# Performance work log

Hardware: AMD Instinct MI355X
Metric: run time of the kernel (lower is better)

Reference implementation:

```python
import jax, jax.numpy as jnp
import numpy as np

H = 8           # attention heads
SPARSITY = 0.5  # fraction of keys kept per query row

def _silu(x):
    return x * jax.nn.sigmoid(x)

def _forward(x_t, t, te_w1, te_b1, te_w2, te_b2, fe_w1, fe_b1, fe_w2, fe_b2,
             fp_w1, fp_b1, fp_w2, fp_b2, fp_w3, fp_b3, fid_emb,
             wq, bq, wk, bk, wv, bv, wo, bo,
             gp_w1, gp_b1, gp_w2, gp_b2, ln_g, ln_b,
             dn_w1, dn_b1, dn_w2, dn_b2, dn_w3, dn_b3):
    B, F = x_t.shape
    D = te_w1.shape[1]
    hd = D // H
    # time / feature embeddings (Linear-SiLU-Linear)
    t_emb = _silu(t[:, None] @ te_w1 + te_b1) @ te_w2 + te_b2        # [B, D]
    x_emb = _silu(x_t @ fe_w1 + fe_b1) @ fe_w2 + fe_b2               # [B, D]
    comb = jnp.concatenate([
        jnp.broadcast_to(x_emb[:, None, :], (B, F, D)),
        jnp.broadcast_to(t_emb[:, None, :], (B, F, D))], axis=-1)    # [B, F, 2D]
    # shared per-feature processor (n_features > 32 branch)
    h = _silu(comb @ fp_w1 + fp_b1)
    h = _silu(h @ fp_w2 + fp_b2)
    h = h @ fp_w3 + fp_b3                                            # [B, F, D]
    d4 = fid_emb.shape[1]
    fid_pad = jnp.concatenate([fid_emb, jnp.zeros((F, D - d4), h.dtype)], axis=-1)
    feats = h + 0.1 * fid_pad[None]                                  # [B, F, D]
    # sparse feature attention (dropout is identity in eval)
    def split(x):
        return x.reshape(B, F, H, hd).transpose(0, 2, 1, 3)          # [B, H, F, hd]
    q = split(feats @ wq + bq)
    k = split(feats @ wk + bk)
    v = split(feats @ wv + bv)
    scores = jnp.einsum('bhqd,bhkd->bhqk', q, k) / (hd ** 0.5)
    k_value = max(1, int(F * SPARSITY))
    thr = jax.lax.top_k(scores, k_value)[0][..., -1:]                # kth largest per row
    scores = jnp.where(scores < thr, -1e9, scores)                   # masked_fill(-1e9)
    attn = jax.nn.softmax(scores, axis=-1)
    out = jnp.einsum('bhqk,bhkd->bhqd', attn, v)
    out = out.transpose(0, 2, 1, 3).reshape(B, F, D) @ wo + bo       # [B, F, D]
    # global pooling + processor with LayerNorm (eps=1e-5)
    g = out.mean(axis=1)
    g = _silu(g @ gp_w1 + gp_b1) @ gp_w2 + gp_b2
    mu = g.mean(-1, keepdims=True)
    var = ((g - mu) ** 2).mean(-1, keepdims=True)
    g = (g - mu) / jnp.sqrt(var + 1e-5) * ln_g + ln_b
    # denoise net -> tanh of mean half
    r = _silu(g @ dn_w1 + dn_b1)
    r = _silu(r @ dn_w2 + dn_b2)
    r = r @ dn_w3 + dn_b3                                            # [B, 2F]
    return jnp.tanh(r[:, :F])

def setup_inputs():
    B, F, D = 512, 128, 512
    D4 = D // 4
    ks = iter(jax.random.split(jax.random.key(0), 40))
    def w(shape):
        return jax.random.normal(next(ks), shape, jnp.float32) / np.sqrt(shape[0]).astype(np.float32)
    z = lambda n: jnp.zeros((n,), jnp.float32)
    return dict(
        x_t=jax.random.normal(next(ks), (B, F), jnp.float32),
        t=jax.random.uniform(next(ks), (B,), jnp.float32),
        te_w1=w((1, D)), te_b1=z(D), te_w2=w((D, D)), te_b2=z(D),
        fe_w1=w((F, D)), fe_b1=z(D), fe_w2=w((D, D)), fe_b2=z(D),
        fp_w1=w((2 * D, D)), fp_b1=z(D), fp_w2=w((D, D)), fp_b2=z(D),
        fp_w3=w((D, D)), fp_b3=z(D),
        fid_emb=jax.random.normal(next(ks), (F, D4), jnp.float32),
        wq=w((D, D)), bq=z(D), wk=w((D, D)), bk=z(D),
        wv=w((D, D)), bv=z(D), wo=w((D, D)), bo=z(D),
        gp_w1=w((D, 2 * D)), gp_b1=z(2 * D), gp_w2=w((2 * D, D)), gp_b2=z(D),
        ln_g=jnp.ones((D,), jnp.float32), ln_b=z(D),
        dn_w1=w((D, 2 * D)), dn_b1=z(2 * D), dn_w2=w((2 * D, 2 * D)), dn_b2=z(2 * D),
        dn_w3=w((2 * D, 2 * F)), dn_b3=z(2 * F),
    )

def reference(x_t, t, te_w1, te_b1, te_w2, te_b2, fe_w1, fe_b1, fe_w2, fe_b2,
              fp_w1, fp_b1, fp_w2, fp_b2, fp_w3, fp_b3, fid_emb,
              wq, bq, wk, bk, wv, bv, wo, bo,
              gp_w1, gp_b1, gp_w2, gp_b2, ln_g, ln_b,
              dn_w1, dn_b1, dn_w2, dn_b2, dn_w3, dn_b3):
    return _forward(x_t, t, te_w1, te_b1, te_w2, te_b2, fe_w1, fe_b1, fe_w2, fe_b2,
                    fp_w1, fp_b1, fp_w2, fp_b2, fp_w3, fp_b3, fid_emb,
                    wq, bq, wk, bk, wv, bv, wo, bo,
                    gp_w1, gp_b1, gp_w2, gp_b2, ln_g, ln_b,
                    dn_w1, dn_b1, dn_w2, dn_b2, dn_w3, dn_b3)
```

## Files before the change

kernel.cpp:

```cpp
#include <hip/hip_runtime.h>

__device__ __forceinline__ float silu_f(float x) { return x / (1.f + __expf(-x)); }

struct AOp {
  const float* P;
  const float* w1;
  const float* b0;
  int lda;
  int tgen;
};

template <int NPROB, int T1GEN>
__global__ __launch_bounds__(256) void gemm_p(
    AOp a0, AOp a1,
    const float* __restrict__ B0, const float* __restrict__ B1,
    const float* __restrict__ B2, int ldb,
    float* __restrict__ O0, float* __restrict__ O1, float* __restrict__ O2,
    int ldc, int Kslab, int ls, long slabMN) {
  __shared__ float As[2][32][68];
  __shared__ float Bs[2][32][68];
  const int tid = threadIdx.x;
  const int z = blockIdx.z;
  const int zi = (NPROB > 1) ? (z >> ls) : 0;
  const int s  = (NPROB > 1) ? (z & ((1 << ls) - 1)) : z;
  const AOp a = (NPROB > 1 && zi == 1) ? a1 : a0;
  const float* Bp = ((NPROB > 2 && zi == 2) ? B2 : (zi == 1) ? B1 : B0)
                    + (long)(s * Kslab) * ldb;
  float* Obase = ((NPROB > 2 && zi == 2) ? O2 : (zi == 1) ? O1 : O0)
                 + (long)s * slabMN;
  const int kbase = s * Kslab;
  const long bm = blockIdx.y * 64, bn = blockIdx.x * 64;
  const int tg = T1GEN ? a.tgen : 0;

  float acc[4][4] = {};
  const int ar = tid >> 3;
  const int ak = (tid & 7) << 2;
  const int br = tid >> 4;
  const int bn4 = (tid & 15) << 2;
  const int ty = tid >> 4, tx = tid & 15;

  float4 rA[2];
  float4 rB[2];
  float4 rW, rC;
  float tm0 = 0.f, tm1 = 0.f;

  auto loadA = [&](int k0) {
    int kg = kbase + k0 + ak;
    if (T1GEN && tg) {
      rW = *(const float4*)&a.w1[kg];
      rC = *(const float4*)&a.b0[kg];
    } else {
#pragma unroll
      for (int h = 0; h < 2; ++h)
        rA[h] = *(const float4*)&a.P[(bm + ar + h * 32) * (long)a.lda + kg];
    }
  };
  auto loadB = [&](int k0) {
#pragma unroll
    for (int h = 0; h < 2; ++h)
      rB[h] = *(const float4*)&Bp[(long)(k0 + br + h * 16) * ldb + bn + bn4];
  };
  auto store = [&](int buf) {
#pragma unroll
    for (int h = 0; h < 2; ++h) {
      int m = ar + h * 32;
      float4 av;
      if (T1GEN && tg) {
        float tm = h ? tm1 : tm0;
        av.x = silu_f(tm * rW.x + rC.x);
        av.y = silu_f(tm * rW.y + rC.y);
        av.z = silu_f(tm * rW.z + rC.z);
        av.w = silu_f(tm * rW.w + rC.w);
      } else {
        av = rA[h];
      }
      As[buf][ak + 0][m] = av.x; As[buf][ak + 1][m] = av.y;
      As[buf][ak + 2][m] = av.z; As[buf][ak + 3][m] = av.w;
    }
#pragma unroll
    for (int h = 0; h < 2; ++h) *(float4*)&Bs[buf][br + h * 16][bn4] = rB[h];
  };

  if (T1GEN && tg) { tm0 = a.P[bm + ar]; tm1 = a.P[bm + ar + 32]; }
  loadA(0); loadB(0);
  store(0);
  if (32 < Kslab) { loadA(32); loadB(32); }

  int cur = 0;
  for (int k0 = 0; k0 < Kslab; k0 += 32) {
    __syncthreads();
    if (k0 + 32 < Kslab) store(cur ^ 1);
    if (k0 + 64 < Kslab) { loadA(k0 + 64); loadB(k0 + 64); }
#pragma unroll
    for (int k = 0; k < 32; ++k) {
      float4 a4 = *(const float4*)&As[cur][k][ty << 2];
      float4 b4 = *(const float4*)&Bs[cur][k][tx << 2];
      float am[4] = {a4.x, a4.y, a4.z, a4.w};
      float bv[4] = {b4.x, b4.y, b4.z, b4.w};
#pragma unroll
      for (int i = 0; i < 4; ++i)
#pragma unroll
        for (int j = 0; j < 4; ++j) acc[i][j] = fmaf(am[i], bv[j], acc[i][j]);
    }
    cur ^= 1;
  }

  float* O = Obase + (bm + ty * 4) * (long)ldc + bn + tx * 4;
#pragma unroll
  for (int i = 0; i < 4; ++i) {
    float4 v = {acc[i][0], acc[i][1], acc[i][2], acc[i][3]};
    *(float4*)&O[(long)i * ldc] = v;
  }
}

__global__ __launch_bounds__(256) void gemm_bt(
    const float* __restrict__ A, int lda, const float* __restrict__ B, int ldb,
    float* __restrict__ OUT, int ldc, int K, float alpha,
    int zAoff, int zBoff, int zCoff) {
  __shared__ float As[2][32][68];
  __shared__ float Bs[2][32][68];
  const int tid = threadIdx.x;
  const int z = blockIdx.z;
  const long bm = blockIdx.y * 64, bn = blockIdx.x * 64;
  const float* Ab = A + (long)z * zAoff;
  const float* Bp = B + (long)z * zBoff;
  float* Obase = OUT + (long)z * zCoff;
  float acc[4][4] = {};
  const int ar = tid >> 3;
  const int ak = (tid & 7) << 2;
  const int ty = tid >> 4, tx = tid & 15;
  float4 rA[2], rB[2];
  auto loadAB = [&](int k0) {
#pragma unroll
    for (int h = 0; h < 2; ++h) {
      rA[h] = *(const float4*)&Ab[(bm + ar + h * 32) * (long)lda + k0 + ak];
      rB[h] = *(const float4*)&Bp[(bn + ar + h * 32) * (long)ldb + k0 + ak];
    }
  };
  auto store = [&](int buf) {
#pragma unroll
    for (int h = 0; h < 2; ++h) {
      int m = ar + h * 32;
      As[buf][ak + 0][m] = rA[h].x; As[buf][ak + 1][m] = rA[h].y;
      As[buf][ak + 2][m] = rA[h].z; As[buf][ak + 3][m] = rA[h].w;
      Bs[buf][ak + 0][m] = rB[h].x; Bs[buf][ak + 1][m] = rB[h].y;
      Bs[buf][ak + 2][m] = rB[h].z; Bs[buf][ak + 3][m] = rB[h].w;
    }
  };
  loadAB(0); store(0);
  if (32 < K) loadAB(32);
  int cur = 0;
  for (int k0 = 0; k0 < K; k0 += 32) {
    __syncthreads();
    if (k0 + 32 < K) store(cur ^ 1);
    if (k0 + 64 < K) loadAB(k0 + 64);
#pragma unroll
    for (int k = 0; k < 32; ++k) {
      float4 a4 = *(const float4*)&As[cur][k][ty << 2];
      float4 b4 = *(const float4*)&Bs[cur][k][tx << 2];
      float am[4] = {a4.x, a4.y, a4.z, a4.w};
      float bv[4] = {b4.x, b4.y, b4.z, b4.w};
#pragma unroll
      for (int i = 0; i < 4; ++i)
#pragma unroll
        for (int j = 0; j < 4; ++j) acc[i][j] = fmaf(am[i], bv[j], acc[i][j]);
    }
    cur ^= 1;
  }
  float* O = Obase + (bm + ty * 4) * (long)ldc + bn + tx * 4;
#pragma unroll
  for (int i = 0; i < 4; ++i) {
    float4 v = {alpha * acc[i][0], alpha * acc[i][1], alpha * acc[i][2],
                alpha * acc[i][3]};
    *(float4*)&O[(long)i * ldc] = v;
  }
}

template <int NS, int ACT>
__global__ __launch_bounds__(256) void sumk(
    const float* __restrict__ P, long slabMN,
    const float* __restrict__ b0, const float* __restrict__ b1, int bsplit,
    int cmask, float* __restrict__ out) {
  int i4 = (blockIdx.x * 256 + threadIdx.x) << 2;
  float4 s = *(const float4*)&P[i4];
#pragma unroll
  for (int si = 1; si < NS; ++si) {
    float4 p = *(const float4*)&P[(long)si * slabMN + i4];
    s.x += p.x; s.y += p.y; s.z += p.z; s.w += p.w;
  }
  int c = i4 & cmask;
  const float* bp = (b1 && c >= bsplit) ? (b1 + c - bsplit) : (b0 + c);
  float4 bb = *(const float4*)bp;
  s.x += bb.x; s.y += bb.y; s.z += bb.z; s.w += bb.w;
  if (ACT == 1) {
    s.x = silu_f(s.x); s.y = silu_f(s.y); s.z = silu_f(s.z); s.w = silu_f(s.w);
  }
  *(float4*)&out[i4] = s;
}

__global__ __launch_bounds__(256) void reduce_tanh(
    const float* __restrict__ P, int slabMN, int nslab,
    const float* __restrict__ bias, float* __restrict__ C) {
  int i4 = (blockIdx.x * 256 + threadIdx.x) << 2;
  float4 s = *(const float4*)&P[i4];
  for (int si = 1; si < nslab; ++si) {
    float4 p = *(const float4*)&P[(long)si * slabMN + i4];
    s.x += p.x; s.y += p.y; s.z += p.z; s.w += p.w;
  }
  int c = i4 & 127;
  float4 v = {tanhf(s.x + bias[c]), tanhf(s.y + bias[c + 1]),
              tanhf(s.z + bias[c + 2]), tanhf(s.w + bias[c + 3])};
  *(float4*)&C[i4] = v;
}

__global__ __launch_bounds__(256) void attn_kernel(
    const float* __restrict__ PBq,
    const float* __restrict__ bq,
    const float* __restrict__ bv,
    const float* __restrict__ kf,
    const float* __restrict__ Mm,
    const float* __restrict__ vf,
    float* __restrict__ pool) {
  const int b = blockIdx.x, h = blockIdx.y;
  const int tid = threadIdx.x;
  __shared__ float uq[64];
  __shared__ float uls[128];
  __shared__ float wpart[4][128];
  __shared__ float wcol[128];
  __shared__ float ppart[2][64];

  if (tid < 64) {
    int c = h * 64 + tid;
    long o = (long)b * 512 + c;
    uq[tid] = PBq[o] + PBq[262144 + o] + PBq[524288 + o] + PBq[786432 + o] + bq[c];
  }
  __syncthreads();
  if (tid < 128) {
    const float* kr = kf + (long)tid * 512 + h * 64;
    float acc = 0.f;
#pragma unroll
    for (int d4 = 0; d4 < 16; ++d4) {
      float4 kv = *(const float4*)&kr[d4 * 4];
      acc += uq[d4 * 4] * kv.x + uq[d4 * 4 + 1] * kv.y +
             uq[d4 * 4 + 2] * kv.z + uq[d4 * 4 + 3] * kv.w;
    }
    uls[tid] = 0.0125f * acc;
  }
  __syncthreads();

  const int lane = tid & 63;
  const int wave = tid >> 6;
  const float u0 = uls[lane], u1 = uls[lane + 64];

  float blo = -0.5f, bhi = 0.5f;
#pragma unroll
  for (int it = 0; it < 11; ++it) {
    float mid = 0.5f * (blo + bhi);
    int n = __popcll(__ballot(u0 >= mid)) + __popcll(__ballot(u1 >= mid));
    bool ge = (n >= 64);
    blo = ge ? mid : blo;
    bhi = ge ? bhi : mid;
  }
  const float wlo = blo - 0.014f, whi = blo + 0.014f;

  float wc0 = 0.f, wc1 = 0.f;
  const float* Mh = Mm + h * 128;
  const int i0 = wave * 32;
  float a0r = Mh[(long)i0 * 1024 + lane];
  float a1r = Mh[(long)i0 * 1024 + lane + 64];
  float b0r = Mh[(long)(i0 + 1) * 1024 + lane];
  float b1r = Mh[(long)(i0 + 1) * 1024 + lane + 64];
  for (int r = 0; r < 32; r += 2) {
    float TA0 = u0 + a0r, TA1 = u1 + a1r;
    float TB0 = u0 + b0r, TB1 = u1 + b1r;
    if (r < 30) {
      a0r = Mh[(long)(i0 + r + 2) * 1024 + lane];
      a1r = Mh[(long)(i0 + r + 2) * 1024 + lane + 64];
      b0r = Mh[(long)(i0 + r + 3) * 1024 + lane];
      b1r = Mh[(long)(i0 + r + 3) * 1024 + lane + 64];
    }
    float loA = wlo, hiA = whi, loB = wlo, hiB = whi;
#pragma unroll
    for (int it = 0; it < 5; ++it) {
      float midA = 0.5f * (loA + hiA), midB = 0.5f * (loB + hiB);
      int nA = __popcll(__ballot(TA0 >= midA)) + __popcll(__ballot(TA1 >= midA));
      int nB = __popcll(__ballot(TB0 >= midB)) + __popcll(__ballot(TB1 >= midB));
      bool gA = (nA >= 64), gB = (nB >= 64);
      loA = gA ? midA : loA; hiA = gA ? hiA : midA;
      loB = gB ? midB : loB; hiB = gB ? hiB : midB;
    }
    float pA0 = (TA0 >= loA) ? __expf(TA0 - loA) : 0.f;
    float pA1 = (TA1 >= loA) ? __expf(TA1 - loA) : 0.f;
    float pB0 = (TB0 >= loB) ? __expf(TB0 - loB) : 0.f;
    float pB1 = (TB1 >= loB) ? __expf(TB1 - loB) : 0.f;
    float sA = pA0 + pA1, sB = pB0 + pB1;
#pragma unroll
    for (int d = 1; d < 64; d <<= 1) {
      sA += __shfl_xor(sA, d);
      sB += __shfl_xor(sB, d);
    }
    float ivA = 1.f / sA, ivB = 1.f / sB;
    wc0 += pA0 * ivA + pB0 * ivB;
    wc1 += pA1 * ivA + pB1 * ivB;
  }
  wpart[wave][lane] = wc0;
  wpart[wave][lane + 64] = wc1;
  __syncthreads();
  if (tid < 128) {
    wcol[tid] = (wpart[0][tid] + wpart[1][tid] + wpart[2][tid] + wpart[3][tid]) *
                (1.f / 128.f);
  }
  __syncthreads();
  if (wave < 2) {
    int j0 = wave * 64;
    const float* vfp = vf + h * 64 + lane;
    float acc = 0.f;
#pragma unroll 8
    for (int jj = 0; jj < 64; ++jj) acc += wcol[j0 + jj] * vfp[(long)(j0 + jj) * 512];
    ppart[wave][lane] = acc;
  }
  __syncthreads();
  if (tid < 64) {
    int d = tid;
    int c = h * 64 + d;
    long o = (long)b * 512 + c;
    long vb0 = 4 * 262144;
    float v = PBq[vb0 + o] + PBq[vb0 + 262144 + o] + PBq[vb0 + 524288 + o] +
              PBq[vb0 + 786432 + o] + bv[c];
    pool[o] = 0.1f * (ppart[0][d] + ppart[1][d]) + v;
  }
}

template <int NSLAB>
__global__ __launch_bounds__(256) void ln_kernel(const float* __restrict__ P,
                                                 const float* __restrict__ bias,
                                                 const float* __restrict__ g,
                                                 const float* __restrict__ bb,
                                                 float* __restrict__ Y) {
  int row = blockIdx.x;
  int tid = threadIdx.x;
  long o0 = (long)row * 512 + tid;
  long o1 = o0 + 256;
  float v0 = bias[tid], v1 = bias[tid + 256];
#pragma unroll
  for (int s = 0; s < NSLAB; ++s) {
    v0 += P[(long)s * 262144 + o0];
    v1 += P[(long)s * 262144 + o1];
  }
  float s = v0 + v1;
#pragma unroll
  for (int d = 1; d < 64; d <<= 1) s += __shfl_xor(s, d);
  __shared__ float r1[4], r2[4];
  if ((tid & 63) == 0) r1[tid >> 6] = s;
  __syncthreads();
  float mean = (r1[0] + r1[1] + r1[2] + r1[3]) * (1.f / 512.f);
  float d0 = v0 - mean, d1 = v1 - mean;
  float q = d0 * d0 + d1 * d1;
#pragma unroll
  for (int d = 1; d < 64; d <<= 1) q += __shfl_xor(q, d);
  if ((tid & 63) == 0) r2[tid >> 6] = q;
  __syncthreads();
  float var = (r2[0] + r2[1] + r2[2] + r2[3]) * (1.f / 512.f);
  float inv = rsqrtf(var + 1e-5f);
  Y[(long)row * 512 + tid] = d0 * inv * g[tid] + bb[tid];
  Y[(long)row * 512 + tid + 256] = d1 * inv * g[tid + 256] + bb[tid + 256];
}


extern "C" void kernel_launch(void* const* d_in, const int* in_sizes, int n_in,
                              void* d_out, int out_size, void* d_ws, size_t ws_size,
                              hipStream_t stream) {
  const float* x_t = (const float*)d_in[0];
  const float* t_in = (const float*)d_in[1];
  const float* te_w1 = (const float*)d_in[2];
  const float* te_b1 = (const float*)d_in[3];
  const float* te_w2 = (const float*)d_in[4];
  const float* te_b2 = (const float*)d_in[5];
  const float* fe_w1 = (const float*)d_in[6];
  const float* fe_b1 = (const float*)d_in[7];
  const float* fe_w2 = (const float*)d_in[8];
  const float* fe_b2 = (const float*)d_in[9];
  const float* fp_w1 = (const float*)d_in[10];
  const float* fp_b1 = (const float*)d_in[11];
  const float* fp_w2 = (const float*)d_in[12];
  const float* fp_b2 = (const float*)d_in[13];
  const float* fp_w3 = (const float*)d_in[14];
  const float* fp_b3 = (const float*)d_in[15];
  const float* fid = (const float*)d_in[16];
  const float* wq = (const float*)d_in[17];
  const float* bq = (const float*)d_in[18];
  const float* wk = (const float*)d_in[19];
  const float* wv = (const float*)d_in[21];
  const float* bv = (const float*)d_in[22];
  const float* wo = (const float*)d_in[23];
  const float* bo = (const float*)d_in[24];
  const float* gp_w1 = (const float*)d_in[25];
  const float* gp_b1 = (const float*)d_in[26];
  const float* gp_w2 = (const float*)d_in[27];
  const float* gp_b2 = (const float*)d_in[28];
  const float* ln_g = (const float*)d_in[29];
  const float* ln_b = (const float*)d_in[30];
  const float* dn_w1 = (const float*)d_in[31];
  const float* dn_b1 = (const float*)d_in[32];
  const float* dn_w2 = (const float*)d_in[33];
  const float* dn_b2 = (const float*)d_in[34];
  const float* dn_w3 = (const float*)d_in[35];
  const float* dn_b3 = (const float*)d_in[36];

  float* W = (float*)d_ws;
  float* P  = W;
  float* XC = W + 2097152;
  float* SA = W + 2621440;
  float* SB = W + 2883584;
  float* qf = W + 3145728;
  float* kf = W + 3211264;
  float* vf = W + 3276800;
  float* Mb = W + 3342336;

  auto ap = [](const float* Pm, int lda) {
    AOp a; a.P = Pm; a.w1 = nullptr; a.b0 = nullptr; a.lda = lda; a.tgen = 0;
    return a;
  };

  gemm_p<3, 0><<<dim3(8, 2, 3), 256, 0, stream>>>(
      ap(fid, 128), ap(fid, 128), wq, wk, wv, 512, qf, kf, vf, 512, 128, 0, 0);
  gemm_bt<<<dim3(2, 2, 8), 256, 0, stream>>>(qf, 512, kf, 512, Mb, 1024, 64,
                                             0.00125f, 64, 64, 128);
  gemm_p<1, 0><<<dim3(8, 8, 4), 256, 0, stream>>>(
      ap(x_t, 128), ap(x_t, 128), fe_w1, nullptr, nullptr, 512,
      P, nullptr, nullptr, 512, 32, 0, 262144);
  sumk<4, 1><<<256, 256, 0, stream>>>(P, 262144, fe_b1, nullptr, 0, 511, SA);
  {
    AOp a1; a1.P = t_in; a1.w1 = te_w1; a1.b0 = te_b1; a1.lda = 0; a1.tgen = 1;
    gemm_p<2, 1><<<dim3(8, 8, 8), 256, 0, stream>>>(
        ap(SA, 512), a1, fe_w2, te_w2, nullptr, 512,
        P, P + 512, nullptr, 1024, 128, 2, 524288);
  }
  sumk<4, 0><<<512, 256, 0, stream>>>(P, 524288, fe_b2, te_b2, 512, 1023, XC);
  gemm_p<1, 0><<<dim3(8, 8, 8), 256, 0, stream>>>(
      ap(XC, 1024), ap(XC, 1024), fp_w1, nullptr, nullptr, 512,
      P, nullptr, nullptr, 512, 128, 0, 262144);
  sumk<8, 1><<<256, 256, 0, stream>>>(P, 262144, fp_b1, nullptr, 0, 511, SB);
  gemm_p<1, 0><<<dim3(8, 8, 8), 256, 0, stream>>>(
      ap(SB, 512), ap(SB, 512), fp_w2, nullptr, nullptr, 512,
      P, nullptr, nullptr, 512, 64, 0, 262144);
  sumk<8, 1><<<256, 256, 0, stream>>>(P, 262144, fp_b2, nullptr, 0, 511, SA);
  gemm_p<1, 0><<<dim3(8, 8, 8), 256, 0, stream>>>(
      ap(SA, 512), ap(SA, 512), fp_w3, nullptr, nullptr, 512,
      P, nullptr, nullptr, 512, 64, 0, 262144);
  sumk<8, 0><<<256, 256, 0, stream>>>(P, 262144, fp_b3, nullptr, 0, 511, SB);
  gemm_p<2, 0><<<dim3(8, 8, 8), 256, 0, stream>>>(
      ap(SB, 512), ap(SB, 512), wq, wv, nullptr, 512,
      P, P + 1048576, nullptr, 512, 128, 2, 262144);
  attn_kernel<<<dim3(512, 8), 256, 0, stream>>>(P, bq, bv, kf, Mb, vf, SA);
  gemm_p<1, 0><<<dim3(8, 8, 8), 256, 0, stream>>>(
      ap(SA, 512), ap(SA, 512), wo, nullptr, nullptr, 512,
      P, nullptr, nullptr, 512, 64, 0, 262144);
  sumk<8, 0><<<256, 256, 0, stream>>>(P, 262144, bo, nullptr, 0, 511, SB);
  gemm_p<1, 0><<<dim3(16, 8, 4), 256, 0, stream>>>(
      ap(SB, 512), ap(SB, 512), gp_w1, nullptr, nullptr, 1024,
      P, nullptr, nullptr, 1024, 128, 0, 524288);
  sumk<4, 1><<<512, 256, 0, stream>>>(P, 524288, gp_b1, nullptr, 0, 1023, XC);
  gemm_p<1, 0><<<dim3(8, 8, 8), 256, 0, stream>>>(
      ap(XC, 1024), ap(XC, 1024), gp_w2, nullptr, nullptr, 512,
      P, nullptr, nullptr, 512, 128, 0, 262144);
  ln_kernel<8><<<512, 256, 0, stream>>>(P, gp_b2, ln_g, ln_b, SA);
  gemm_p<1, 0><<<dim3(16, 8, 4), 256, 0, stream>>>(
      ap(SA, 512), ap(SA, 512), dn_w1, nullptr, nullptr, 1024,
      P, nullptr, nullptr, 1024, 128, 0, 524288);
  sumk<4, 1><<<512, 256, 0, stream>>>(P, 524288, dn_b1, nullptr, 0, 1023, XC);
  gemm_p<1, 0><<<dim3(16, 8, 4), 256, 0, stream>>>(
      ap(XC, 1024), ap(XC, 1024), dn_w2, nullptr, nullptr, 1024,
      P, nullptr, nullptr, 1024, 256, 0, 524288);
  sumk<4, 1><<<512, 256, 0, stream>>>(P, 524288, dn_b2, nullptr, 0, 1023, XC);
  gemm_p<1, 0><<<dim3(2, 8, 16), 256, 0, stream>>>(
      ap(XC, 1024), ap(XC, 1024), dn_w3, nullptr, nullptr, 256,
      P, nullptr, nullptr, 128, 64, 0, 65536);
  reduce_tanh<<<64, 256, 0, stream>>>(P, 65536, 16, dn_b3, (float*)d_out);
}
```

Before: 288.0 us.

## Fold embedding second layers into fp_w1 and merge prologue GEMMs into two kernels

The second linear layers of the feature and time embeddings (fe_w2, te_w2) are pre-multiplied into fp_w1, giving effective weights Wx and Wt and a combined bias beff1. This removes one full B×512×1024 GEMM stage and its reduction kernel, and the x-embedding no longer has to be materialised. The small prologue GEMMs (fid QKV, the QK^T score bias, fe_w1, the weight products, the bias fold and the first reduction) are packed into two multi-role kernels, pre1 and pre2, built on a shared device GEMM routine, which cuts launches. The trade-off is extra weight-by-weight GEMM work on every call and a different floating-point summation order.

```diff
diff --git a/kernel.cpp b/kernel.cpp
--- a/kernel.cpp
+++ b/kernel.cpp
@@ -2,70 +2,50 @@
 
 __device__ __forceinline__ float silu_f(float x) { return x / (1.f + __expf(-x)); }
 
-struct AOp {
-  const float* P;
-  const float* w1;
-  const float* b0;
-  int lda;
-  int tgen;
-};
-
-template <int NPROB, int T1GEN>
-__global__ __launch_bounds__(256) void gemm_p(
-    AOp a0, AOp a1,
-    const float* __restrict__ B0, const float* __restrict__ B1,
-    const float* __restrict__ B2, int ldb,
-    float* __restrict__ O0, float* __restrict__ O1, float* __restrict__ O2,
-    int ldc, int Kslab, int ls, long slabMN) {
-  __shared__ float As[2][32][68];
-  __shared__ float Bs[2][32][68];
+template <int TG, int BT>
+__device__ __forceinline__ void dev_gemm(
+    float (*As)[32][68], float (*Bs)[32][68],
+    const float* __restrict__ Ap, int lda,
+    const float* __restrict__ tw1, const float* __restrict__ tb0,
+    const float* __restrict__ Bp, int ldb,
+    float* __restrict__ Obase, int ldc,
+    int kbase, int Kslab, long bm, long bn, float alpha) {
   const int tid = threadIdx.x;
-  const int z = blockIdx.z;
-  const int zi = (NPROB > 1) ? (z >> ls) : 0;
-  const int s  = (NPROB > 1) ? (z & ((1 << ls) - 1)) : z;
-  const AOp a = (NPROB > 1 && zi == 1) ? a1 : a0;
-  const float* Bp = ((NPROB > 2 && zi == 2) ? B2 : (zi == 1) ? B1 : B0)
-                    + (long)(s * Kslab) * ldb;
-  float* Obase = ((NPROB > 2 && zi == 2) ? O2 : (zi == 1) ? O1 : O0)
-                 + (long)s * slabMN;
-  const int kbase = s * Kslab;
-  const long bm = blockIdx.y * 64, bn = blockIdx.x * 64;
-  const int tg = T1GEN ? a.tgen : 0;
-
+  const int ar = tid >> 3, ak = (tid & 7) << 2;
+  const int br = tid >> 4, bn4 = (tid & 15) << 2;
+  const int ty = tid >> 4, tx = tid & 15;
   float acc[4][4] = {};
-  const int ar = tid >> 3;
-  const int ak = (tid & 7) << 2;
-  const int br = tid >> 4;
-  const int bn4 = (tid & 15) << 2;
-  const int ty = tid >> 4, tx = tid & 15;
-
-  float4 rA[2];
-  float4 rB[2];
-  float4 rW, rC;
+  float4 rA[2], rB[2], rW, rC;
   float tm0 = 0.f, tm1 = 0.f;
-
+  if (TG) { tm0 = Ap[bm + ar]; tm1 = Ap[bm + ar + 32]; }
   auto loadA = [&](int k0) {
     int kg = kbase + k0 + ak;
-    if (T1GEN && tg) {
-      rW = *(const float4*)&a.w1[kg];
-      rC = *(const float4*)&a.b0[kg];
+    if (TG) {
+      rW = *(const float4*)&tw1[kg];
+      rC = *(const float4*)&tb0[kg];
     } else {
 #pragma unroll
       for (int h = 0; h < 2; ++h)
-        rA[h] = *(const float4*)&a.P[(bm + ar + h * 32) * (long)a.lda + kg];
+        rA[h] = *(const float4*)&Ap[(bm + ar + h * 32) * (long)lda + kg];
     }
   };
   auto loadB = [&](int k0) {
-#pragma unroll
-    for (int h = 0; h < 2; ++h)
-      rB[h] = *(const float4*)&Bp[(long)(k0 + br + h * 16) * ldb + bn + bn4];
+    if (BT) {
+#pragma unroll
+      for (int h = 0; h < 2; ++h)
+        rB[h] = *(const float4*)&Bp[(bn + ar + h * 32) * (long)ldb + kbase + k0 + ak];
+    } else {
+#pragma unroll
+      for (int h = 0; h < 2; ++h)
+        rB[h] = *(const float4*)&Bp[(long)(k0 + br + h * 16) * ldb + bn + bn4];
+    }
   };
   auto store = [&](int buf) {
 #pragma unroll
     for (int h = 0; h < 2; ++h) {
       int m = ar + h * 32;
       float4 av;
-      if (T1GEN && tg) {
+      if (TG) {
         float tm = h ? tm1 : tm0;
         av.x = silu_f(tm * rW.x + rC.x);
         av.y = silu_f(tm * rW.y + rC.y);
@@ -77,15 +57,21 @@
       As[buf][ak + 0][m] = av.x; As[buf][ak + 1][m] = av.y;
       As[buf][ak + 2][m] = av.z; As[buf][ak + 3][m] = av.w;
     }
-#pragma unroll
-    for (int h = 0; h < 2; ++h) *(float4*)&Bs[buf][br + h * 16][bn4] = rB[h];
+    if (BT) {
+#pragma unroll
+      for (int h = 0; h < 2; ++h) {
+        int n = ar + h * 32;
+        Bs[buf][ak + 0][n] = rB[h].x; Bs[buf][ak + 1][n] = rB[h].y;
+        Bs[buf][ak + 2][n] = rB[h].z; Bs[buf][ak + 3][n] = rB[h].w;
+      }
+    } else {
+#pragma unroll
+      for (int h = 0; h < 2; ++h) *(float4*)&Bs[buf][br + h * 16][bn4] = rB[h];
+    }
   };
-
-  if (T1GEN && tg) { tm0 = a.P[bm + ar]; tm1 = a.P[bm + ar + 32]; }
   loadA(0); loadB(0);
   store(0);
   if (32 < Kslab) { loadA(32); loadB(32); }
-
   int cur = 0;
   for (int k0 = 0; k0 < Kslab; k0 += 32) {
     __syncthreads();
@@ -104,69 +90,6 @@
     }
     cur ^= 1;
   }
-
-  float* O = Obase + (bm + ty * 4) * (long)ldc + bn + tx * 4;
-#pragma unroll
-  for (int i = 0; i < 4; ++i) {
-    float4 v = {acc[i][0], acc[i][1], acc[i][2], acc[i][3]};
-    *(float4*)&O[(long)i * ldc] = v;
-  }
-}
-
-__global__ __launch_bounds__(256) void gemm_bt(
-    const float* __restrict__ A, int lda, const float* __restrict__ B, int ldb,
-    float* __restrict__ OUT, int ldc, int K, float alpha,
-    int zAoff, int zBoff, int zCoff) {
-  __shared__ float As[2][32][68];
-  __shared__ float Bs[2][32][68];
-  const int tid = threadIdx.x;
-  const int z = blockIdx.z;
-  const long bm = blockIdx.y * 64, bn = blockIdx.x * 64;
-  const float* Ab = A + (long)z * zAoff;
-  const float* Bp = B + (long)z * zBoff;
-  float* Obase = OUT + (long)z * zCoff;
-  float acc[4][4] = {};
-  const int ar = tid >> 3;
-  const int ak = (tid & 7) << 2;
-  const int ty = tid >> 4, tx = tid & 15;
-  float4 rA[2], rB[2];
-  auto loadAB = [&](int k0) {
-#pragma unroll
-    for (int h = 0; h < 2; ++h) {
-      rA[h] = *(const float4*)&Ab[(bm + ar + h * 32) * (long)lda + k0 + ak];
-      rB[h] = *(const float4*)&Bp[(bn + ar + h * 32) * (long)ldb + k0 + ak];
-    }
-  };
-  auto store = [&](int buf) {
-#pragma unroll
-    for (int h = 0; h < 2; ++h) {
-      int m = ar + h * 32;
-      As[buf][ak + 0][m] = rA[h].x; As[buf][ak + 1][m] = rA[h].y;
-      As[buf][ak + 2][m] = rA[h].z; As[buf][ak + 3][m] = rA[h].w;
-      Bs[buf][ak + 0][m] = rB[h].x; Bs[buf][ak + 1][m] = rB[h].y;
-      Bs[buf][ak + 2][m] = rB[h].z; Bs[buf][ak + 3][m] = rB[h].w;
-    }
-  };
-  loadAB(0); store(0);
-  if (32 < K) loadAB(32);
-  int cur = 0;
-  for (int k0 = 0; k0 < K; k0 += 32) {
-    __syncthreads();
-    if (k0 + 32 < K) store(cur ^ 1);
-    if (k0 + 64 < K) loadAB(k0 + 64);
-#pragma unroll
-    for (int k = 0; k < 32; ++k) {
-      float4 a4 = *(const float4*)&As[cur][k][ty << 2];
-      float4 b4 = *(const float4*)&Bs[cur][k][tx << 2];
-      float am[4] = {a4.x, a4.y, a4.z, a4.w};
-      float bv[4] = {b4.x, b4.y, b4.z, b4.w};
-#pragma unroll
-      for (int i = 0; i < 4; ++i)
-#pragma unroll
-        for (int j = 0; j < 4; ++j) acc[i][j] = fmaf(am[i], bv[j], acc[i][j]);
-    }
-    cur ^= 1;
-  }
   float* O = Obase + (bm + ty * 4) * (long)ldc + bn + tx * 4;
 #pragma unroll
   for (int i = 0; i < 4; ++i) {
@@ -176,11 +99,123 @@
   }
 }
 
+struct AOp {
+  const float* P;
+  const float* w1;
+  const float* b0;
+  int lda;
+  int tgen;
+};
+
+template <int NPROB, int T1GEN>
+__global__ __launch_bounds__(256) void gemm_p(
+    AOp a0, AOp a1,
+    const float* __restrict__ B0, const float* __restrict__ B1,
+    const float* __restrict__ B2, int ldb,
+    float* __restrict__ O0, float* __restrict__ O1, float* __restrict__ O2,
+    int ldc, int Kslab, int ls, long slabMN) {
+  __shared__ float As[2][32][68];
+  __shared__ float Bs[2][32][68];
+  const int z = blockIdx.z;
+  const int zi = (NPROB > 1) ? (z >> ls) : 0;
+  const int s = (NPROB > 1) ? (z & ((1 << ls) - 1)) : z;
+  const AOp a = (NPROB > 1 && zi == 1) ? a1 : a0;
+  const float* Bp = ((NPROB > 2 && zi == 2) ? B2 : (zi == 1) ? B1 : B0)
+                    + (long)(s * Kslab) * ldb;
+  float* Obase = ((NPROB > 2 && zi == 2) ? O2 : (zi == 1) ? O1 : O0)
+                 + (long)s * slabMN;
+  const int kbase = s * Kslab;
+  const long bm = blockIdx.y * 64, bn = blockIdx.x * 64;
+  if (T1GEN && a.tgen)
+    dev_gemm<1, 0>(As, Bs, a.P, 0, a.w1, a.b0, Bp, ldb, Obase, ldc, kbase,
+                   Kslab, bm, bn, 1.f);
+  else
+    dev_gemm<0, 0>(As, Bs, a.P, a.lda, nullptr, nullptr, Bp, ldb, Obase, ldc,
+                   kbase, Kslab, bm, bn, 1.f);
+}
+
+__global__ __launch_bounds__(256) void pre1(
+    const float* fid, const float* wq, const float* wk, const float* wv,
+    const float* x_t, const float* fe_w1,
+    const float* fe_w2, const float* te_w2, const float* fp_w1,
+    float* qf, float* kf, float* vf, float* P, float* Wx, float* Wt) {
+  __shared__ float As[2][32][68];
+  __shared__ float Bs[2][32][68];
+  const int w = blockIdx.x;
+  if (w < 48) {
+    int prob = w >> 4, t = w & 15;
+    const float* B = prob == 0 ? wq : (prob == 1 ? wk : wv);
+    float* O = prob == 0 ? qf : (prob == 1 ? kf : vf);
+    dev_gemm<0, 0>(As, Bs, fid, 128, nullptr, nullptr, B, 512, O, 512, 0, 128,
+                   (t >> 3) * 64, (t & 7) * 64, 1.f);
+  } else if (w < 304) {
+    int w2 = w - 48, s = w2 & 3, t = w2 >> 2;
+    dev_gemm<0, 0>(As, Bs, x_t, 128, nullptr, nullptr,
+                   fe_w1 + (long)(s * 32) * 512, 512, P + (long)s * 262144, 512,
+                   s * 32, 32, (t >> 3) * 64, (t & 7) * 64, 1.f);
+  } else if (w < 368) {
+    int t = w - 304;
+    dev_gemm<0, 0>(As, Bs, fe_w2, 512, nullptr, nullptr, fp_w1, 512, Wx, 512,
+                   0, 512, (t >> 3) * 64, (t & 7) * 64, 1.f);
+  } else {
+    int t = w - 368;
+    dev_gemm<0, 0>(As, Bs, te_w2, 512, nullptr, nullptr,
+                   fp_w1 + (long)512 * 512, 512, Wt, 512, 0, 512,
+                   (t >> 3) * 64, (t & 7) * 64, 1.f);
+  }
+}
+
+__global__ __launch_bounds__(256) void pre2(
+    const float* qf, const float* kf, float* Mb,
+    const float* fp_b1, const float* fe_b2, const float* te_b2,
+    const float* fp_w1, float* beff1,
+    const float* P, const float* fe_b1, float* SA) {
+  __shared__ float As[2][32][68];
+  __shared__ float Bs[2][32][68];
+  __shared__ float red[4][64];
+  const int w = blockIdx.x;
+  const int tid = threadIdx.x;
+  if (w < 32) {
+    int h = w >> 2, t = w & 3;
+    dev_gemm<0, 1>(As, Bs, qf + h * 64, 512, nullptr, nullptr, kf + h * 64, 512,
+                   Mb + h * 128, 1024, 0, 64, (t >> 1) * 64, (t & 1) * 64,
+                   0.00125f);
+  } else if (w < 40) {
+    int w2 = w - 32;
+    int c = w2 * 64 + (tid & 63);
+    int ks = tid >> 6;
+    float acc = 0.f;
+    for (int k = ks * 128; k < ks * 128 + 128; ++k)
+      acc += fe_b2[k] * fp_w1[(long)k * 512 + c] +
+             te_b2[k] * fp_w1[(long)(512 + k) * 512 + c];
+    red[ks][tid & 63] = acc;
+    __syncthreads();
+    if (tid < 64)
+      beff1[w2 * 64 + tid] =
+          fp_b1[w2 * 64 + tid] + red[0][tid] + red[1][tid] + red[2][tid] + red[3][tid];
+  } else {
+    int idx0 = (w - 40) * 256 + tid;
+    for (int q = 0; q < 4; ++q) {
+      long i4 = (long)(idx0 + q * 16384) << 2;
+      float4 s = *(const float4*)&P[i4];
+#pragma unroll
+      for (int si = 1; si < 4; ++si) {
+        float4 p = *(const float4*)&P[(long)si * 262144 + i4];
+        s.x += p.x; s.y += p.y; s.z += p.z; s.w += p.w;
+      }
+      int c = (int)i4 & 511;
+      float4 bb = *(const float4*)&fe_b1[c];
+      s.x = silu_f(s.x + bb.x); s.y = silu_f(s.y + bb.y);
+      s.z = silu_f(s.z + bb.z); s.w = silu_f(s.w + bb.w);
+      *(float4*)&SA[i4] = s;
+    }
+  }
+}
+
 template <int NS, int ACT>
 __global__ __launch_bounds__(256) void sumk(
     const float* __restrict__ P, long slabMN,
-    const float* __restrict__ b0, const float* __restrict__ b1, int bsplit,
-    int cmask, float* __restrict__ out) {
+    const float* __restrict__ b0, int cmask, float* __restrict__ out) {
   int i4 = (blockIdx.x * 256 + threadIdx.x) << 2;
   float4 s = *(const float4*)&P[i4];
 #pragma unroll
@@ -189,8 +224,7 @@
     s.x += p.x; s.y += p.y; s.z += p.z; s.w += p.w;
   }
   int c = i4 & cmask;
-  const float* bp = (b1 && c >= bsplit) ? (b1 + c - bsplit) : (b0 + c);
-  float4 bb = *(const float4*)bp;
+  float4 bb = *(const float4*)&b0[c];
   s.x += bb.x; s.y += bb.y; s.z += bb.z; s.w += bb.w;
   if (ACT == 1) {
     s.x = silu_f(s.x); s.y = silu_f(s.y); s.z = silu_f(s.z); s.w = silu_f(s.w);
@@ -214,12 +248,9 @@
 }
 
 __global__ __launch_bounds__(256) void attn_kernel(
-    const float* __restrict__ PBq,
-    const float* __restrict__ bq,
-    const float* __restrict__ bv,
-    const float* __restrict__ kf,
-    const float* __restrict__ Mm,
-    const float* __restrict__ vf,
+    const float* __restrict__ PBq, const float* __restrict__ bq,
+    const float* __restrict__ bv, const float* __restrict__ kf,
+    const float* __restrict__ Mm, const float* __restrict__ vf,
     float* __restrict__ pool) {
   const int b = blockIdx.x, h = blockIdx.y;
   const int tid = threadIdx.x;
@@ -331,7 +362,6 @@
   }
 }
 
-template <int NSLAB>
 __global__ __launch_bounds__(256) void ln_kernel(const float* __restrict__ P,
                                                  const float* __restrict__ bias,
                                                  const float* __restrict__ g,
@@ -343,7 +373,7 @@
   long o1 = o0 + 256;
   float v0 = bias[tid], v1 = bias[tid + 256];
 #pragma unroll
-  for (int s = 0; s < NSLAB; ++s) {
+  for (int s = 0; s < 8; ++s) {
     v0 += P[(long)s * 262144 + o0];
     v1 += P[(long)s * 262144 + o1];
   }
@@ -365,7 +395,6 @@
   Y[(long)row * 512 + tid] = d0 * inv * g[tid] + bb[tid];
   Y[(long)row * 512 + tid + 256] = d1 * inv * g[tid + 256] + bb[tid + 256];
 }
-
 
 extern "C" void kernel_launch(void* const* d_in, const int* in_sizes, int n_in,
                               void* d_out, int out_size, void* d_ws, size_t ws_size,
@@ -408,47 +437,43 @@
   const float* dn_b3 = (const float*)d_in[36];
 
   float* W = (float*)d_ws;
-  float* P  = W;
-  float* XC = W + 2097152;
-  float* SA = W + 2621440;
-  float* SB = W + 2883584;
-  float* qf = W + 3145728;
-  float* kf = W + 3211264;
-  float* vf = W + 3276800;
-  float* Mb = W + 3342336;
+  float* P   = W;
+  float* XC  = W + 2097152;
+  float* SB  = W + 2621440;
+  float* SA  = W + 2883584;
+  float* XC2 = W + 2621440;
+  float* Wx  = W + 3145728;
+  float* Wt  = W + 3407872;
+  float* qf  = W + 3670016;
+  float* kf  = W + 3735552;
+  float* vf  = W + 3801088;
+  float* Mb  = W + 3866624;
+  float* beff1 = W + 3997696;
 
   auto ap = [](const float* Pm, int lda) {
     AOp a; a.P = Pm; a.w1 = nullptr; a.b0 = nullptr; a.lda = lda; a.tgen = 0;
     return a;
   };
 
-  gemm_p<3, 0><<<dim3(8, 2, 3), 256, 0, stream>>>(
-      ap(fid, 128), ap(fid, 128), wq, wk, wv, 512, qf, kf, vf, 512, 128, 0, 0);
-  gemm_bt<<<dim3(2, 2, 8), 256, 0, stream>>>(qf, 512, kf, 512, Mb, 1024, 64,
-                                             0.00125f, 64, 64, 128);
-  gemm_p<1, 0><<<dim3(8, 8, 4), 256, 0, stream>>>(
-      ap(x_t, 128), ap(x_t, 128), fe_w1, nullptr, nullptr, 512,
-      P, nullptr, nullptr, 512, 32, 0, 262144);
-  sumk<4, 1><<<256, 256, 0, stream>>>(P, 262144, fe_b1, nullptr, 0, 511, SA);
+  pre1<<<432, 256, 0, stream>>>(fid, wq, wk, wv, x_t, fe_w1, fe_w2, te_w2,
+                                fp_w1, qf, kf, vf, P, Wx, Wt);
+  pre2<<<104, 256, 0, stream>>>(qf, kf, Mb, fp_b1, fe_b2, te_b2, fp_w1, beff1,
+                                P, fe_b1, SA);
   {
     AOp a1; a1.P = t_in; a1.w1 = te_w1; a1.b0 = te_b1; a1.lda = 0; a1.tgen = 1;
     gemm_p<2, 1><<<dim3(8, 8, 8), 256, 0, stream>>>(
-        ap(SA, 512), a1, fe_w2, te_w2, nullptr, 512,
-        P, P + 512, nullptr, 1024, 128, 2, 524288);
-  }
-  sumk<4, 0><<<512, 256, 0, stream>>>(P, 524288, fe_b2, te_b2, 512, 1023, XC);
-  gemm_p<1, 0><<<dim3(8, 8, 8), 256, 0, stream>>>(
-      ap(XC, 1024), ap(XC, 1024), fp_w1, nullptr, nullptr, 512,
-      P, nullptr, nullptr, 512, 128, 0, 262144);
-  sumk<8, 1><<<256, 256, 0, stream>>>(P, 262144, fp_b1, nullptr, 0, 511, SB);
+        ap(SA, 512), a1, Wx, Wt, nullptr, 512,
+        P, P + 1048576, nullptr, 512, 128, 2, 262144);
+  }
+  sumk<8, 1><<<256, 256, 0, stream>>>(P, 262144, beff1, 511, SB);
   gemm_p<1, 0><<<dim3(8, 8, 8), 256, 0, stream>>>(
       ap(SB, 512), ap(SB, 512), fp_w2, nullptr, nullptr, 512,
       P, nullptr, nullptr, 512, 64, 0, 262144);
-  sumk<8, 1><<<256, 256, 0, stream>>>(P, 262144, fp_b2, nullptr, 0, 511, SA);
+  sumk<8, 1><<<256, 256, 0, stream>>>(P, 262144, fp_b2, 511, SA);
   gemm_p<1, 0><<<dim3(8, 8, 8), 256, 0, stream>>>(
       ap(SA, 512), ap(SA, 512), fp_w3, nullptr, nullptr, 512,
       P, nullptr, nullptr, 512, 64, 0, 262144);
-  sumk<8, 0><<<256, 256, 0, stream>>>(P, 262144, fp_b3, nullptr, 0, 511, SB);
+  sumk<8, 0><<<256, 256, 0, stream>>>(P, 262144, fp_b3, 511, SB);
   gemm_p<2, 0><<<dim3(8, 8, 8), 256, 0, stream>>>(
       ap(SB, 512), ap(SB, 512), wq, wv, nullptr, 512,
       P, P + 1048576, nullptr, 512, 128, 2, 262144);
@@ -456,25 +481,25 @@
   gemm_p<1, 0><<<dim3(8, 8, 8), 256, 0, stream>>>(
       ap(SA, 512), ap(SA, 512), wo, nullptr, nullptr, 512,
       P, nullptr, nullptr, 512, 64, 0, 262144);
-  sumk<8, 0><<<256, 256, 0, stream>>>(P, 262144, bo, nullptr, 0, 511, SB);
+  sumk<8, 0><<<256, 256, 0, stream>>>(P, 262144, bo, 511, SB);
   gemm_p<1, 0><<<dim3(16, 8, 4), 256, 0, stream>>>(
       ap(SB, 512), ap(SB, 512), gp_w1, nullptr, nullptr, 1024,
       P, nullptr, nullptr, 1024, 128, 0, 524288);
-  sumk<4, 1><<<512, 256, 0, stream>>>(P, 524288, gp_b1, nullptr, 0, 1023, XC);
+  sumk<4, 1><<<512, 256, 0, stream>>>(P, 524288, gp_b1, 1023, XC);
   gemm_p<1, 0><<<dim3(8, 8, 8), 256, 0, stream>>>(
       ap(XC, 1024), ap(XC, 1024), gp_w2, nullptr, nullptr, 512,
       P, nullptr, nullptr, 512, 128, 0, 262144);
-  ln_kernel<8><<<512, 256, 0, stream>>>(P, gp_b2, ln_g, ln_b, SA);
+  ln_kernel<<<512, 256, 0, stream>>>(P, gp_b2, ln_g, ln_b, SA);
   gemm_p<1, 0><<<dim3(16, 8, 4), 256, 0, stream>>>(
       ap(SA, 512), ap(SA, 512), dn_w1, nullptr, nullptr, 1024,
       P, nullptr, nullptr, 1024, 128, 0, 524288);
-  sumk<4, 1><<<512, 256, 0, stream>>>(P, 524288, dn_b1, nullptr, 0, 1023, XC);
+  sumk<4, 1><<<512, 256, 0, stream>>>(P, 524288, dn_b1, 1023, XC);
   gemm_p<1, 0><<<dim3(16, 8, 4), 256, 0, stream>>>(
       ap(XC, 1024), ap(XC, 1024), dn_w2, nullptr, nullptr, 1024,
       P, nullptr, nullptr, 1024, 256, 0, 524288);
-  sumk<4, 1><<<512, 256, 0, stream>>>(P, 524288, dn_b2, nullptr, 0, 1023, XC);
+  sumk<4, 1><<<512, 256, 0, stream>>>(P, 524288, dn_b2, 1023, XC2);
   gemm_p<1, 0><<<dim3(2, 8, 16), 256, 0, stream>>>(
-      ap(XC, 1024), ap(XC, 1024), dn_w3, nullptr, nullptr, 256,
+      ap(XC2, 1024), ap(XC2, 1024), dn_w3, nullptr, nullptr, 256,
       P, nullptr, nullptr, 128, 64, 0, 65536);
   reduce_tanh<<<64, 256, 0, stream>>>(P, 65536, 16, dn_b3, (float*)d_out);
 }
```

Measured after the change: 282.6 us. About the same (-1.9%).
